# Optimization experiments

Measured on AMD Instinct MI355X. Metric: run time of the kernel, lower is better.

The kernel has to match this reference:

```python
import jax, jax.numpy as jnp
import numpy as np

EPS = 1e-06

def setup_inputs() -> dict:
    key = jax.random.key(0)
    kq, kk, kv = jax.random.split(key, 3)
    shape = (8, 16, 4096, 64)  # [B, H, N, D]
    q = jax.random.normal(kq, shape, dtype=jnp.float32)
    k = jax.random.normal(kk, shape, dtype=jnp.float32)
    v = jax.random.normal(kv, shape, dtype=jnp.float32)
    return {"q": q, "k": k, "v": v}

def reference(q, k, v):
    # softmax over sequence axis (n) for keys, over feature axis (d) for queries
    k_sm = jax.nn.softmax(k, axis=-2)   # [B,H,N,D]
    q_sm = jax.nn.softmax(q, axis=-1)   # [B,H,N,D]
    # context: [B,H,D,E] -- avoids the NxN attention matrix
    context = jnp.einsum('bhnd,bhne->bhde', k_sm, v)
    denom = jnp.sum(k_sm, axis=-2)[..., :, None] + EPS  # [B,H,D,1]
    context = context / denom
    out = jnp.einsum('bhnd,bhde->bhne', q_sm, context)  # [B,H,N,E]
    # dropout p=0.0 / eval mode -> identity
    return out
```

## Files before the change

kernel.cpp:

```cpp
#include <hip/hip_runtime.h>
#include <cstddef>
#include <cstdint>

#define BHN 128
#define NSEQ 4096
#define EPSF 1e-6f

constexpr int K2_S = 8;
constexpr int K2_ROWS = NSEQ / K2_S;
constexpr int K2_TILE = 64;
constexpr int K2_TILES = K2_ROWS / K2_TILE;

__global__ __launch_bounds__(256, 4)
void k2_partial_ctx(const float* __restrict__ K, const float* __restrict__ V,
                    float* __restrict__ part_ctx, float* __restrict__ part_cs)
{
    __shared__ __align__(16) float ke[K2_TILE * 64];
    __shared__ __align__(16) float vs[K2_TILE * 64];

    const int bh  = blockIdx.x;
    const int s   = blockIdx.y;
    const int tid = threadIdx.x;
    const int w    = tid >> 6;
    const int lane = tid & 63;
    const int l8   = lane & 7;
    const int h8   = lane >> 3;

    const float4* Kg = (const float4*)(K + ((size_t)bh * NSEQ + (size_t)s * K2_ROWS) * 64);
    const float4* Vg = (const float4*)(V + ((size_t)bh * NSEQ + (size_t)s * K2_ROWS) * 64);

    float acc[8][8];
    #pragma unroll
    for (int i = 0; i < 8; ++i)
        #pragma unroll
        for (int j = 0; j < 8; ++j) acc[i][j] = 0.f;
    float cs[8];
    #pragma unroll
    for (int i = 0; i < 8; ++i) cs[i] = 0.f;

    for (int t = 0; t < K2_TILES; ++t) {
        const float4* kt = Kg + t * (K2_TILE * 16);
        const float4* vt = Vg + t * (K2_TILE * 16);
        float4* ke4 = (float4*)ke;
        float4* vs4 = (float4*)vs;
        #pragma unroll
        for (int p = 0; p < 4; ++p) {
            const int f = tid + p * 256;
            float4 kq = kt[f];
            kq.x = __expf(kq.x);
            kq.y = __expf(kq.y);
            kq.z = __expf(kq.z);
            kq.w = __expf(kq.w);
            ke4[f] = kq;
            vs4[f] = vt[f];
        }
        __syncthreads();
        const float4* keR = (const float4*)ke;
        const float4* vsR = (const float4*)vs;
        #pragma unroll
        for (int nn = 0; nn < 16; ++nn) {
            const int n = w * 16 + nn;
            float4 a0 = keR[n * 16 + h8];
            float4 a1 = keR[n * 16 + 8 + h8];
            float4 b0 = vsR[n * 16 + l8];
            float4 b1 = vsR[n * 16 + 8 + l8];
            float a[8] = {a0.x, a0.y, a0.z, a0.w, a1.x, a1.y, a1.z, a1.w};
            float b[8] = {b0.x, b0.y, b0.z, b0.w, b1.x, b1.y, b1.z, b1.w};
            #pragma unroll
            for (int i = 0; i < 8; ++i) cs[i] += a[i];
            #pragma unroll
            for (int i = 0; i < 8; ++i)
                #pragma unroll
                for (int j = 0; j < 8; ++j)
                    acc[i][j] = fmaf(a[i], b[j], acc[i][j]);
        }
        __syncthreads();
    }

    float* red   = vs;
    float* redcs = ke;
    for (int wv = 0; wv < 4; ++wv) {
        if (w == wv) {
            #pragma unroll
            for (int i = 0; i < 8; ++i) {
                const int d = (i < 4) ? (4 * h8 + i) : (32 + 4 * h8 + (i - 4));
                #pragma unroll
                for (int ej = 0; ej < 2; ++ej) {
                    float4* dst = (float4*)&red[d * 64 + ej * 32 + 4 * l8];
                    float4 vv = make_float4(acc[i][4*ej+0], acc[i][4*ej+1],
                                            acc[i][4*ej+2], acc[i][4*ej+3]);
                    if (wv == 0) {
                        *dst = vv;
                    } else {
                        float4 o = *dst;
                        o.x += vv.x; o.y += vv.y; o.z += vv.z; o.w += vv.w;
                        *dst = o;
                    }
                }
                if (l8 == 0) {
                    if (wv == 0) redcs[d] = cs[i];
                    else         redcs[d] += cs[i];
                }
            }
        }
        __syncthreads();
    }

    float4* pc = (float4*)(part_ctx + (size_t)(bh * K2_S + s) * 4096);
    const float4* red4 = (const float4*)red;
    #pragma unroll
    for (int p = 0; p < 4; ++p) {
        const int f = tid + p * 256;
        pc[f] = red4[f];
    }
    if (tid < 16) {
        ((float4*)(part_cs + (size_t)(bh * K2_S + s) * 64))[tid] =
            ((const float4*)redcs)[tid];
    }
}

__global__ __launch_bounds__(256)
void k2_reduce(const float* __restrict__ part_ctx, const float* __restrict__ part_cs,
               float* __restrict__ ctxf)
{
    __shared__ float inv_cs[64];
    const int bh  = blockIdx.x;
    const int tid = threadIdx.x;
    if (tid < 64) {
        float c = 0.f;
        #pragma unroll
        for (int s = 0; s < K2_S; ++s)
            c += part_cs[(size_t)(bh * K2_S + s) * 64 + tid];
        inv_cs[tid] = 1.0f / (c * (1.0f + EPSF));
    }
    __syncthreads();
    const float4* pc = (const float4*)(part_ctx + (size_t)bh * K2_S * 4096);
    float4* cf = (float4*)(ctxf + (size_t)bh * 4096);
    const int f = blockIdx.y * 256 + tid;
    float4 sum = make_float4(0.f, 0.f, 0.f, 0.f);
    #pragma unroll
    for (int s = 0; s < K2_S; ++s) {
        float4 x = pc[s * 1024 + f];
        sum.x += x.x; sum.y += x.y; sum.z += x.z; sum.w += x.w;
    }
    const float inv = inv_cs[f >> 4];
    sum.x *= inv; sum.y *= inv; sum.z *= inv; sum.w *= inv;
    cf[f] = sum;
}

constexpr int K3_ROWS  = 128;
constexpr int QSTRIDE  = 68;

__global__ __launch_bounds__(256, 3)
void k3_out(const float* __restrict__ Q, const float* __restrict__ ctxf,
            float* __restrict__ out)
{
    __shared__ __align__(16) float qe[K3_ROWS * QSTRIDE];
    __shared__ __align__(16) float ctx_s[4096];
    __shared__ float rs[K3_ROWS];

    const int bh  = blockIdx.x;
    const int n0  = blockIdx.y * K3_ROWS;
    const int tid = threadIdx.x;
    const int w    = tid >> 6;
    const int lane = tid & 63;
    const int l8   = lane & 7;
    const int h8   = lane >> 3;

    {
        const float4* cg = (const float4*)(ctxf + (size_t)bh * 4096);
        float4* cs4 = (float4*)ctx_s;
        #pragma unroll
        for (int p = 0; p < 4; ++p)
            cs4[tid + p * 256] = cg[tid + p * 256];
    }
    {
        const float4* qg = (const float4*)(Q + ((size_t)bh * NSEQ + n0) * 64);
        const int rgrp = tid >> 4;
        const int c4   = tid & 15;
        #pragma unroll
        for (int p = 0; p < 8; ++p) {
            const int rr = p * 16 + rgrp;
            float4 x = qg[rr * 16 + c4];
            x.x = __expf(x.x); x.y = __expf(x.y);
            x.z = __expf(x.z); x.w = __expf(x.w);
            float ssum = x.x + x.y + x.z + x.w;
            ssum += __shfl_xor(ssum, 1);
            ssum += __shfl_xor(ssum, 2);
            ssum += __shfl_xor(ssum, 4);
            ssum += __shfl_xor(ssum, 8);
            if (c4 == 0) rs[rr] = ssum;
            *(float4*)(qe + rr * QSTRIDE + 4 * c4) = x;
        }
    }
    __syncthreads();

    int rowi[4];
    #pragma unroll
    for (int i = 0; i < 4; ++i) rowi[i] = 32 * w + 8 * i + h8;

    float acc[4][8];
    #pragma unroll
    for (int i = 0; i < 4; ++i)
        #pragma unroll
        for (int j = 0; j < 8; ++j) acc[i][j] = 0.f;

    for (int dc = 0; dc < 64; dc += 4) {
        float a[4][4];
        #pragma unroll
        for (int i = 0; i < 4; ++i) {
            float4 aq = *(const float4*)(qe + rowi[i] * QSTRIDE + dc);
            a[i][0] = aq.x; a[i][1] = aq.y; a[i][2] = aq.z; a[i][3] = aq.w;
        }
        float b[4][8];
        #pragma unroll
        for (int dd = 0; dd < 4; ++dd) {
            float4 b0 = *(const float4*)(ctx_s + (dc + dd) * 64 + 4 * l8);
            float4 b1 = *(const float4*)(ctx_s + (dc + dd) * 64 + 32 + 4 * l8);
            b[dd][0] = b0.x; b[dd][1] = b0.y; b[dd][2] = b0.z; b[dd][3] = b0.w;
            b[dd][4] = b1.x; b[dd][5] = b1.y; b[dd][6] = b1.z; b[dd][7] = b1.w;
        }
        #pragma unroll
        for (int dd = 0; dd < 4; ++dd)
            #pragma unroll
            for (int i = 0; i < 4; ++i)
                #pragma unroll
                for (int j = 0; j < 8; ++j)
                    acc[i][j] = fmaf(a[i][dd], b[dd][j], acc[i][j]);
    }

    float4* og = (float4*)(out + ((size_t)bh * NSEQ + n0) * 64);
    #pragma unroll
    for (int i = 0; i < 4; ++i) {
        const float inv = 1.0f / rs[rowi[i]];
        #pragma unroll
        for (int ej = 0; ej < 2; ++ej) {
            float4 vv = make_float4(acc[i][4*ej+0]*inv, acc[i][4*ej+1]*inv,
                                    acc[i][4*ej+2]*inv, acc[i][4*ej+3]*inv);
            og[rowi[i] * 16 + ej * 8 + l8] = vv;
        }
    }
}

extern "C" void kernel_launch(void* const* d_in, const int* in_sizes, int n_in,
                              void* d_out, int out_size, void* d_ws, size_t ws_size,
                              hipStream_t stream)
{
    const float* q = (const float*)d_in[0];
    const float* k = (const float*)d_in[1];
    const float* v = (const float*)d_in[2];
    float* out = (float*)d_out;

    float* part_ctx = (float*)d_out;
    float* part_cs  = (float*)d_ws;
    float* ctxf     = part_cs + (size_t)1024 * 64;

    k2_partial_ctx<<<dim3(BHN, K2_S), 256, 0, stream>>>(k, v, part_ctx, part_cs);
    k2_reduce<<<dim3(BHN, 4), 256, 0, stream>>>(part_ctx, part_cs, ctxf);
    k3_out<<<dim3(BHN, NSEQ / K3_ROWS), 256, 0, stream>>>(q, ctxf, out);
}
```

Baseline: 457.0 us.

## Double-buffer K/V tiles with async global-to-LDS loads for V

Halves the tile to 32 rows and double-buffers the K and V shared tiles. The next tile is prefetched while the current one is computed: V goes directly to LDS via global_load_lds, and K goes through registers and is exponentiated after the FMA loop. This aims to hide global load latency behind compute and drop one barrier per tile. In exchange there are more loop iterations, more register pressure from the held K values, and a dependence on the async LDS load ordering, which the single barrier per iteration must cover.

```diff
diff --git a/kernel.cpp b/kernel.cpp
--- a/kernel.cpp
+++ b/kernel.cpp
@@ -8,15 +8,23 @@
 
 constexpr int K2_S = 8;
 constexpr int K2_ROWS = NSEQ / K2_S;
-constexpr int K2_TILE = 64;
+constexpr int K2_TILE = 32;
 constexpr int K2_TILES = K2_ROWS / K2_TILE;
+
+__device__ __forceinline__ void gload_lds16(const void* g, void* l)
+{
+    __builtin_amdgcn_global_load_lds(
+        (const __attribute__((address_space(1))) uint32_t*)g,
+        (__attribute__((address_space(3))) uint32_t*)l,
+        16, 0, 0);
+}
 
 __global__ __launch_bounds__(256, 4)
 void k2_partial_ctx(const float* __restrict__ K, const float* __restrict__ V,
                     float* __restrict__ part_ctx, float* __restrict__ part_cs)
 {
-    __shared__ __align__(16) float ke[K2_TILE * 64];
-    __shared__ __align__(16) float vs[K2_TILE * 64];
+    __shared__ __align__(16) float ke[2][K2_TILE * 64];
+    __shared__ __align__(16) float vs[2][K2_TILE * 64];
 
     const int bh  = blockIdx.x;
     const int s   = blockIdx.y;
@@ -38,28 +46,40 @@
     #pragma unroll
     for (int i = 0; i < 8; ++i) cs[i] = 0.f;
 
+    const int vofs0 = w * 512;
+    const int vofs1 = w * 512 + 256;
+
+    {
+        gload_lds16(Vg + w * 128 + lane,      &vs[0][vofs0]);
+        gload_lds16(Vg + w * 128 + 64 + lane, &vs[0][vofs1]);
+        float4 k0 = Kg[tid];
+        float4 k1 = Kg[tid + 256];
+        k0.x = __expf(k0.x); k0.y = __expf(k0.y); k0.z = __expf(k0.z); k0.w = __expf(k0.w);
+        k1.x = __expf(k1.x); k1.y = __expf(k1.y); k1.z = __expf(k1.z); k1.w = __expf(k1.w);
+        ((float4*)ke[0])[tid]       = k0;
+        ((float4*)ke[0])[tid + 256] = k1;
+    }
+    __syncthreads();
+
+    int cur = 0;
     for (int t = 0; t < K2_TILES; ++t) {
-        const float4* kt = Kg + t * (K2_TILE * 16);
-        const float4* vt = Vg + t * (K2_TILE * 16);
-        float4* ke4 = (float4*)ke;
-        float4* vs4 = (float4*)vs;
-        #pragma unroll
-        for (int p = 0; p < 4; ++p) {
-            const int f = tid + p * 256;
-            float4 kq = kt[f];
-            kq.x = __expf(kq.x);
-            kq.y = __expf(kq.y);
-            kq.z = __expf(kq.z);
-            kq.w = __expf(kq.w);
-            ke4[f] = kq;
-            vs4[f] = vt[f];
-        }
-        __syncthreads();
-        const float4* keR = (const float4*)ke;
-        const float4* vsR = (const float4*)vs;
-        #pragma unroll
-        for (int nn = 0; nn < 16; ++nn) {
-            const int n = w * 16 + nn;
+        const int nxt = cur ^ 1;
+        float4 k0, k1;
+        const bool pf = (t + 1 < K2_TILES);
+        if (pf) {
+            const float4* vt = Vg + (t + 1) * 512;
+            const float4* kt = Kg + (t + 1) * 512;
+            gload_lds16(vt + w * 128 + lane,      &vs[nxt][vofs0]);
+            gload_lds16(vt + w * 128 + 64 + lane, &vs[nxt][vofs1]);
+            k0 = kt[tid];
+            k1 = kt[tid + 256];
+        }
+
+        const float4* keR = (const float4*)ke[cur];
+        const float4* vsR = (const float4*)vs[cur];
+        #pragma unroll
+        for (int nn = 0; nn < 8; ++nn) {
+            const int n = w * 8 + nn;
             float4 a0 = keR[n * 16 + h8];
             float4 a1 = keR[n * 16 + 8 + h8];
             float4 b0 = vsR[n * 16 + l8];
@@ -74,11 +94,19 @@
                 for (int j = 0; j < 8; ++j)
                     acc[i][j] = fmaf(a[i], b[j], acc[i][j]);
         }
+
+        if (pf) {
+            k0.x = __expf(k0.x); k0.y = __expf(k0.y); k0.z = __expf(k0.z); k0.w = __expf(k0.w);
+            k1.x = __expf(k1.x); k1.y = __expf(k1.y); k1.z = __expf(k1.z); k1.w = __expf(k1.w);
+            ((float4*)ke[nxt])[tid]       = k0;
+            ((float4*)ke[nxt])[tid + 256] = k1;
+        }
         __syncthreads();
-    }
-
-    float* red   = vs;
-    float* redcs = ke;
+        cur = nxt;
+    }
+
+    float* red   = &vs[0][0];
+    float* redcs = &ke[0][0];
     for (int wv = 0; wv < 4; ++wv) {
         if (w == wv) {
             #pragma unroll
```

Result: slower. 506.7 us (+10.9%).
